# Performance work log

Hardware: AMD Instinct MI355X
Metric: run time of the kernel (lower is better)

Reference implementation:

```python
import jax, jax.numpy as jnp
import numpy as np

SFREQ = 100
NPERSEG = 100  # min(n_times=200, 100)
NOVERLAP = NPERSEG // 2

# periodic hann window (scipy get_window('hann', N) with sym=False)
_WIN_NP = 0.5 - 0.5 * np.cos(2.0 * np.pi * np.arange(NPERSEG) / NPERSEG)
_WIN_SQ_SUM = float(np.sum(_WIN_NP ** 2))
_FREQS = np.fft.rfftfreq(NPERSEG, 1.0 / SFREQ)  # 0..50 Hz, 51 bins
_BANDS = [(0.5, 4.0), (4.0, 8.0), (8.0, 13.0), (13.0, 30.0)]  # delta/theta/alpha/beta
_BAND_IDX = [np.where((_FREQS >= lo) & (_FREQS <= hi))[0] for lo, hi in _BANDS]


def welch_band_features(x):
    """Batched Welch PSD band powers. x: (B,C,T) -> (B, C*4)."""
    B, C, T = x.shape
    step = NPERSEG - NOVERLAP
    n_seg = (T - NPERSEG) // step + 1
    seg_idx = np.arange(n_seg)[:, None] * step + np.arange(NPERSEG)  # (S, L)
    segs = x[..., seg_idx]                              # (B,C,S,L)
    segs = segs - segs.mean(-1, keepdims=True)          # detrend='constant'
    win = jnp.asarray(_WIN_NP, x.dtype)
    spec = jnp.fft.rfft(segs * win, axis=-1)            # (B,C,S,F)
    scale = 1.0 / (SFREQ * _WIN_SQ_SUM)
    psd = (spec.real ** 2 + spec.imag ** 2) * scale
    psd = psd.at[..., 1:-1].multiply(2.0)               # one-sided, nfft even
    psd = psd.mean(-2)                                  # average over segments -> (B,C,F)
    feats = jnp.stack([psd[..., idx].mean(-1) for idx in _BAND_IDX], axis=-1)  # (B,C,4)
    return feats.reshape(B, C * 4)


def setup_inputs() -> dict:
    key = jax.random.key(0)
    ks = jax.random.split(key, 16)
    B, C, T = 2048, 129, 200
    red = C // 8  # 16
    s = 0.05
    inp = {
        "x": jax.random.normal(ks[0], (B, C, T), jnp.float32),
        # channel attention fc (no bias)
        "w_att1": jax.random.normal(ks[1], (C, red), jnp.float32) * s,
        "w_att2": jax.random.normal(ks[2], (red, C), jnp.float32) * s,
        # stand-in EEGNeX backbone: time-mean pool + linear C->64
        "w_bb": jax.random.normal(ks[3], (C, 64), jnp.float32) * s,
        "b_bb": jnp.zeros((64,), jnp.float32),
        # freq encoder
        "w_fe1": jax.random.normal(ks[4], (C * 4, 128), jnp.float32) * s,
        "b_fe1": jnp.zeros((128,), jnp.float32),
        "w_fe2": jax.random.normal(ks[5], (128, 64), jnp.float32) * s,
        "b_fe2": jnp.zeros((64,), jnp.float32),
        # head
        "w_h1": jax.random.normal(ks[6], (128, 128), jnp.float32) * s,
        "b_h1": jnp.zeros((128,), jnp.float32),
        "w_h2": jax.random.normal(ks[7], (128, 64), jnp.float32) * s,
        "b_h2": jnp.zeros((64,), jnp.float32),
        "w_h3": jax.random.normal(ks[8], (64, 1), jnp.float32) * s,
        "b_h3": jnp.zeros((1,), jnp.float32),
    }
    return inp


def reference(x, w_att1, w_att2, w_bb, b_bb, w_fe1, b_fe1, w_fe2, b_fe2,
              w_h1, b_h1, w_h2, b_h2, w_h3, b_h3):
    # --- channel attention ---
    avg = x.mean(-1)                                    # (B,C)
    mx = x.max(-1)                                      # (B,C)
    fc = lambda v: jax.nn.relu(v @ w_att1) @ w_att2
    att = jax.nn.sigmoid(fc(avg) + fc(mx))[..., None]   # (B,C,1)
    x_att = x * att
    # --- backbone (stand-in for EEGNeXBase): time pool + linear ---
    time_feat = jax.nn.relu(x_att.mean(-1) @ w_bb + b_bb)  # (B,64)
    # --- frequency branch (computed from raw x, detached in original) ---
    freq = welch_band_features(jax.lax.stop_gradient(x))   # (B, C*4)
    freq = jax.nn.relu(freq @ w_fe1 + b_fe1)
    freq = jax.nn.relu(freq @ w_fe2 + b_fe2)               # (B,64)
    # --- head ---
    h = jnp.concatenate([time_feat, freq], axis=1)         # (B,128)
    h = jax.nn.relu(h @ w_h1 + b_h1)
    h = jax.nn.relu(h @ w_h2 + b_h2)
    return h @ w_h3 + b_h3                                  # (B,1)
```

## Files before the change

kernel.cpp:

```cpp
#include <hip/hip_runtime.h>
#include <math.h>

constexpr int BB = 2048;
constexpr int CC = 129;
constexpr int TT = 200;
constexpr int NPAIR = BB * CC;
constexpr int PPB = 64;
constexpr int XSTR = 204;

constexpr int OFF_AVG = 8192;
constexpr int OFF_MX  = OFF_AVG + NPAIR;
constexpr int OFF_FT  = OFF_MX + NPAIR;

typedef __bf16 bf16x8 __attribute__((ext_vector_type(8)));
typedef float  f32x4  __attribute__((ext_vector_type(4)));

union BFU { int4 v; bf16x8 b; };
union BSU { __bf16 b; unsigned short u; };

__global__ void kInit(unsigned short* __restrict__ bfr) {
    int tid = blockIdx.x * 256 + threadIdx.x;
    if (tid >= 16384) return;
    int i    = tid & 7;
    int lane = (tid >> 3) & 63;
    int h    = (tid >> 9) & 1;
    int nt   = (tid >> 10) & 3;
    int ks   = tid >> 12;
    int k = ks * 32 + (lane >> 4) * 8 + i;
    int n = nt * 16 + (lane & 15);
    float v = 0.f;
    if (k < 100) {
        if (n < 60) {
            int kb = (n >> 1) + 1;
            const float C = 0.06283185307179587f;
            float w = 0.5f - 0.5f * cosf(C * (float)k);
            int ph = (kb * k) % 100;
            float ang = C * (float)ph;
            v = w * ((n & 1) ? sinf(ang) : cosf(ang));
        } else if (n == 60) {
            v = 0.01f;
        }
    }
    __bf16 hb = (__bf16)v;
    BSU out;
    if (h == 0) out.b = hb;
    else        out.b = (__bf16)(v - (float)hb);
    bfr[tid] = out.u;
}

__global__ __launch_bounds__(256, 2) void kA(const float* __restrict__ x,
                                             const unsigned short* __restrict__ bfr,
                                             float* __restrict__ avg,
                                             float* __restrict__ mxg,
                                             float* __restrict__ feat) {
    __shared__ __align__(16) float xs[PPB * XSTR + 32];

    const int tid = threadIdx.x;
    const int blk = blockIdx.x;

    {
        const float4* xg = (const float4*)(x + (size_t)blk * PPB * TT);
        #pragma unroll
        for (int it = 0; it < 13; it++) {
            int idx = tid + it * 256;
            if (idx < 3200) {
                float4 v = xg[idx];
                int p = idx / 50, t4 = (idx % 50) * 4;
                *(float4*)(xs + p * XSTR + t4) = v;
            }
        }
        if (tid < 64) *(float4*)(xs + tid * XSTR + 200) = float4{0.f, 0.f, 0.f, 0.f};
        if (tid < 32) xs[PPB * XSTR + tid] = 0.f;
    }

    bf16x8 Bh[4][4], Bl[4][4];
    {
        const int4* bg = (const int4*)bfr;
        int ln = tid & 63;
        #pragma unroll
        for (int ks = 0; ks < 4; ks++)
            #pragma unroll
            for (int nt = 0; nt < 4; nt++) {
                BFU uh, ul;
                uh.v = bg[((ks * 4 + nt) * 2 + 0) * 64 + ln];
                ul.v = bg[((ks * 4 + nt) * 2 + 1) * 64 + ln];
                Bh[ks][nt] = uh.b;
                Bl[ks][nt] = ul.b;
            }
    }
    __syncthreads();

    {
        int p = tid >> 2, q = tid & 3;
        const float* src = xs + p * XSTR + q * 50;
        float m = -3.4e38f;
        #pragma unroll
        for (int i = 0; i < 25; i++) {
            float2 v = *(const float2*)(src + i * 2);
            m = fmaxf(m, fmaxf(v.x, v.y));
        }
        m = fmaxf(m, __shfl_xor(m, 1, 64));
        m = fmaxf(m, __shfl_xor(m, 2, 64));
        if (q == 0) mxg[blk * PPB + p] = m;
    }

    const int wv = tid >> 6, lane = tid & 63;
    const int quad = lane >> 4, mrow = lane & 15;
    f32x4 acc[3][4];
    #pragma unroll
    for (int a = 0; a < 3; a++)
        #pragma unroll
        for (int b = 0; b < 4; b++) acc[a][b] = f32x4{0.f, 0.f, 0.f, 0.f};

    #pragma unroll
    for (int mi = 0; mi < 3; mi++) {
        int mt = wv * 3 + mi;
        int r = mt * 16 + mrow;
        int pair = r / 3;
        int seg = r - pair * 3;
        const float* abase = xs + pair * XSTR + seg * 50 + quad * 8;
        #pragma unroll
        for (int ks = 0; ks < 4; ks++) {
            const float* s = abase + ks * 32;
            float2 f0 = *(const float2*)(s);
            float2 f1 = *(const float2*)(s + 2);
            float2 f2 = *(const float2*)(s + 4);
            float2 f3 = *(const float2*)(s + 6);
            float f[8] = {f0.x, f0.y, f1.x, f1.y, f2.x, f2.y, f3.x, f3.y};
            bf16x8 Ah, Al;
            #pragma unroll
            for (int i = 0; i < 8; i++) {
                __bf16 hb = (__bf16)f[i];
                Ah[i] = hb;
                Al[i] = (__bf16)(f[i] - (float)hb);
            }
            #pragma unroll
            for (int nt = 0; nt < 4; nt++) {
                acc[mi][nt] = __builtin_amdgcn_mfma_f32_16x16x32_bf16(Al, Bh[ks][nt], acc[mi][nt], 0, 0, 0);
                acc[mi][nt] = __builtin_amdgcn_mfma_f32_16x16x32_bf16(Ah, Bl[ks][nt], acc[mi][nt], 0, 0, 0);
                acc[mi][nt] = __builtin_amdgcn_mfma_f32_16x16x32_bf16(Ah, Bh[ks][nt], acc[mi][nt], 0, 0, 0);
            }
        }
    }
    __syncthreads();

    float* sp = xs;
    #pragma unroll
    for (int mi = 0; mi < 3; mi++) {
        int mt = wv * 3 + mi;
        #pragma unroll
        for (int nt = 0; nt < 4; nt++) {
            int col = nt * 16 + mrow;
            #pragma unroll
            for (int i = 0; i < 4; i++) {
                int row = mt * 16 + quad * 4 + i;
                sp[row * 66 + col] = acc[mi][nt][i];
            }
        }
    }
    __syncthreads();

    {
        int p = tid >> 2, bnd = tid & 3;
        const int c0[4] = {0, 6, 14, 24};
        const int c1[4] = {7, 15, 25, 59};
        float sum = 0.f;
        #pragma unroll
        for (int s = 0; s < 3; s++) {
            const float* row = sp + (p * 3 + s) * 66;
            float mu = row[60];
            int lo = c0[bnd];
            if (bnd == 0) {
                float v = row[0] + 25.f * mu;
                sum += v * v;
                lo = 1;
            }
            for (int c = lo; c <= c1[bnd]; c++) {
                float v = row[c];
                sum += v * v;
            }
        }
        if (bnd == 0)
            avg[blk * PPB + p] = (sp[(p * 3) * 66 + 60] + sp[(p * 3 + 2) * 66 + 60]) * 0.5f;
        const float cnt[4] = {4.f, 5.f, 6.f, 18.f};
        feat[(size_t)(blk * PPB + p) * 4 + bnd] = sum * (2.f / (11250.f * cnt[bnd]));
    }
}

__global__ __launch_bounds__(256, 8) void kB(const float* __restrict__ avg,
                                             const float* __restrict__ mxv,
                                             const float* __restrict__ feat,
                                             const float* __restrict__ w_att1,
                                             const float* __restrict__ w_att2,
                                             const float* __restrict__ w_bb,
                                             const float* __restrict__ b_bb,
                                             const float* __restrict__ w_fe1,
                                             const float* __restrict__ b_fe1,
                                             const float* __restrict__ w_fe2,
                                             const float* __restrict__ b_fe2,
                                             const float* __restrict__ w_h1,
                                             const float* __restrict__ b_h1,
                                             const float* __restrict__ w_h2,
                                             const float* __restrict__ b_h2,
                                             const float* __restrict__ w_h3,
                                             const float* __restrict__ b_h3,
                                             float* __restrict__ out) {
    __shared__ float s_avg[132], s_mx[132], s_fq[520];
    __shared__ float s_t1a[16], s_t1b[16], s_t1[16];
    __shared__ float s_v[132];
    __shared__ float s_tf[2][64];
    __shared__ float s_p1[2][128];
    __shared__ float s_f1[128];
    __shared__ float s_p2[4][64];
    __shared__ float s_h[128];
    __shared__ float s_pg1[2][128];
    __shared__ float s_g1[128];
    __shared__ float s_pg2[4][64];

    const int b = blockIdx.x;
    const int tid = threadIdx.x;

    for (int i = tid; i < 129; i += 256) { s_avg[i] = avg[b * 129 + i]; s_mx[i] = mxv[b * 129 + i]; }
    for (int i = tid; i < 516; i += 256) s_fq[i] = feat[(size_t)b * 516 + i];
    __syncthreads();

    if (tid < 32) {
        int h = tid & 15;
        const float* src = (tid >= 16) ? s_mx : s_avg;
        float acc = 0.f;
        #pragma unroll 4
        for (int c = 0; c < 129; c++) acc += src[c] * w_att1[c * 16 + h];
        ((tid >= 16) ? s_t1b : s_t1a)[h] = fmaxf(acc, 0.f);
    }
    __syncthreads();
    if (tid < 16) s_t1[tid] = s_t1a[tid] + s_t1b[tid];
    __syncthreads();

    if (tid < 129) {
        float l = 0.f;
        #pragma unroll
        for (int j = 0; j < 16; j++) l += s_t1[j] * w_att2[j * 129 + tid];
        s_v[tid] = s_avg[tid] / (1.f + expf(-l));
    }
    __syncthreads();

    if (tid < 128) {
        int o = tid & 63, ks = tid >> 6;
        int i0 = ks ? 65 : 0, i1 = ks ? 129 : 65;
        float acc = 0.f;
        #pragma unroll 4
        for (int i = i0; i < i1; i++) acc += s_v[i] * w_bb[i * 64 + o];
        s_tf[ks][o] = acc;
    }
    {
        int o = tid & 127, ks = tid >> 7;
        float acc = 0.f;
        #pragma unroll 4
        for (int i = ks * 258; i < ks * 258 + 258; i++) acc += s_fq[i] * w_fe1[i * 128 + o];
        s_p1[ks][o] = acc;
    }
    __syncthreads();
    if (tid < 64) s_h[tid] = fmaxf(s_tf[0][tid] + s_tf[1][tid] + b_bb[tid], 0.f);
    if (tid >= 128) { int o = tid - 128; s_f1[o] = fmaxf(s_p1[0][o] + s_p1[1][o] + b_fe1[o], 0.f); }
    __syncthreads();

    {
        int o = tid & 63, ks = tid >> 6;
        float acc = 0.f;
        #pragma unroll 4
        for (int i = ks * 32; i < ks * 32 + 32; i++) acc += s_f1[i] * w_fe2[i * 64 + o];
        s_p2[ks][o] = acc;
    }
    __syncthreads();
    if (tid < 64) s_h[64 + tid] = fmaxf(s_p2[0][tid] + s_p2[1][tid] + s_p2[2][tid] + s_p2[3][tid] + b_fe2[tid], 0.f);
    __syncthreads();

    {
        int o = tid & 127, ks = tid >> 7;
        float acc = 0.f;
        #pragma unroll 4
        for (int i = ks * 64; i < ks * 64 + 64; i++) acc += s_h[i] * w_h1[i * 128 + o];
        s_pg1[ks][o] = acc;
    }
    __syncthreads();
    if (tid < 128) s_g1[tid] = fmaxf(s_pg1[0][tid] + s_pg1[1][tid] + b_h1[tid], 0.f);
    __syncthreads();

    {
        int o = tid & 63, ks = tid >> 6;
        float acc = 0.f;
        #pragma unroll 4
        for (int i = ks * 32; i < ks * 32 + 32; i++) acc += s_g1[i] * w_h2[i * 64 + o];
        s_pg2[ks][o] = acc;
    }
    __syncthreads();

    if (tid < 64) {
        float g2 = fmaxf(s_pg2[0][tid] + s_pg2[1][tid] + s_pg2[2][tid] + s_pg2[3][tid] + b_h2[tid], 0.f);
        float pz = g2 * w_h3[tid];
        for (int off = 32; off >= 1; off >>= 1) pz += __shfl_xor(pz, off, 64);
        if (tid == 0) out[b] = pz + b_h3[0];
    }
}

extern "C" void kernel_launch(void* const* d_in, const int* in_sizes, int n_in,
                              void* d_out, int out_size, void* d_ws, size_t ws_size,
                              hipStream_t stream) {
    const float* x      = (const float*)d_in[0];
    const float* w_att1 = (const float*)d_in[1];
    const float* w_att2 = (const float*)d_in[2];
    const float* w_bb   = (const float*)d_in[3];
    const float* b_bb   = (const float*)d_in[4];
    const float* w_fe1  = (const float*)d_in[5];
    const float* b_fe1  = (const float*)d_in[6];
    const float* w_fe2  = (const float*)d_in[7];
    const float* b_fe2  = (const float*)d_in[8];
    const float* w_h1   = (const float*)d_in[9];
    const float* b_h1   = (const float*)d_in[10];
    const float* w_h2   = (const float*)d_in[11];
    const float* b_h2   = (const float*)d_in[12];
    const float* w_h3   = (const float*)d_in[13];
    const float* b_h3   = (const float*)d_in[14];

    float* ws = (float*)d_ws;
    unsigned short* bfr = (unsigned short*)ws;
    float* avg = ws + OFF_AVG;
    float* mxv = ws + OFF_MX;
    float* feat = ws + OFF_FT;

    kInit<<<64, 256, 0, stream>>>(bfr);
    kA<<<NPAIR / PPB, 256, 0, stream>>>(x, bfr, avg, mxv, feat);
    kB<<<BB, 256, 0, stream>>>(avg, mxv, feat,
                               w_att1, w_att2, w_bb, b_bb,
                               w_fe1, b_fe1, w_fe2, b_fe2,
                               w_h1, b_h1, w_h2, b_h2, w_h3, b_h3,
                               (float*)d_out);
}
```

Measured before the change: 478.5 us.

## Make kA wave-independent with per-wave LDS slices and no block barriers

```diff
diff --git a/kernel.cpp b/kernel.cpp
--- a/kernel.cpp
+++ b/kernel.cpp
@@ -7,6 +7,7 @@
 constexpr int NPAIR = BB * CC;
 constexpr int PPB = 64;
 constexpr int XSTR = 204;
+constexpr int WSLICE = 16 * XSTR;
 
 constexpr int OFF_AVG = 8192;
 constexpr int OFF_MX  = OFF_AVG + NPAIR;
@@ -48,85 +49,90 @@
     bfr[tid] = out.u;
 }
 
-__global__ __launch_bounds__(256, 2) void kA(const float* __restrict__ x,
+__global__ __launch_bounds__(256, 3) void kA(const float* __restrict__ x,
                                              const unsigned short* __restrict__ bfr,
                                              float* __restrict__ avg,
                                              float* __restrict__ mxg,
                                              float* __restrict__ feat) {
-    __shared__ __align__(16) float xs[PPB * XSTR + 32];
-
-    const int tid = threadIdx.x;
-    const int blk = blockIdx.x;
-
-    {
-        const float4* xg = (const float4*)(x + (size_t)blk * PPB * TT);
-        #pragma unroll
-        for (int it = 0; it < 13; it++) {
-            int idx = tid + it * 256;
-            if (idx < 3200) {
-                float4 v = xg[idx];
-                int p = idx / 50, t4 = (idx % 50) * 4;
-                *(float4*)(xs + p * XSTR + t4) = v;
-            }
-        }
-        if (tid < 64) *(float4*)(xs + tid * XSTR + 200) = float4{0.f, 0.f, 0.f, 0.f};
-        if (tid < 32) xs[PPB * XSTR + tid] = 0.f;
-    }
-
-    bf16x8 Bh[4][4], Bl[4][4];
-    {
-        const int4* bg = (const int4*)bfr;
-        int ln = tid & 63;
-        #pragma unroll
-        for (int ks = 0; ks < 4; ks++)
-            #pragma unroll
-            for (int nt = 0; nt < 4; nt++) {
-                BFU uh, ul;
-                uh.v = bg[((ks * 4 + nt) * 2 + 0) * 64 + ln];
-                ul.v = bg[((ks * 4 + nt) * 2 + 1) * 64 + ln];
-                Bh[ks][nt] = uh.b;
-                Bl[ks][nt] = ul.b;
-            }
-    }
-    __syncthreads();
-
-    {
-        int p = tid >> 2, q = tid & 3;
-        const float* src = xs + p * XSTR + q * 50;
+    __shared__ __align__(16) float xs[4 * WSLICE];
+
+    const int tid  = threadIdx.x;
+    const int blk  = blockIdx.x;
+    const int wv   = tid >> 6;
+    const int lane = tid & 63;
+
+    float* wx = xs + wv * WSLICE;
+
+    {
+        const int p = lane >> 2, q = lane & 3;
+        const float* rowg = x + ((size_t)blk * PPB + wv * 16 + p) * TT;
+        float* rowl = wx + p * XSTR;
         float m = -3.4e38f;
         #pragma unroll
-        for (int i = 0; i < 25; i++) {
-            float2 v = *(const float2*)(src + i * 2);
-            m = fmaxf(m, fmaxf(v.x, v.y));
+        for (int j = 0; j < 13; j++) {
+            int i4 = q + 4 * j;
+            if (i4 < 50) {
+                float4 v = *(const float4*)(rowg + i4 * 4);
+                *(float4*)(rowl + i4 * 4) = v;
+                m = fmaxf(fmaxf(m, fmaxf(v.x, v.y)), fmaxf(v.z, v.w));
+            }
         }
         m = fmaxf(m, __shfl_xor(m, 1, 64));
         m = fmaxf(m, __shfl_xor(m, 2, 64));
-        if (q == 0) mxg[blk * PPB + p] = m;
-    }
-
-    const int wv = tid >> 6, lane = tid & 63;
+        if (q == 0) mxg[blk * PPB + wv * 16 + p] = m;
+    }
+
     const int quad = lane >> 4, mrow = lane & 15;
+
+    const float* abase[3];
+    {
+        #pragma unroll
+        for (int mi = 0; mi < 3; mi++) {
+            int lr = mi * 16 + mrow;
+            int pl = lr / 3;
+            int sg = lr - pl * 3;
+            abase[mi] = wx + pl * XSTR + sg * 50;
+        }
+    }
+
     f32x4 acc[3][4];
     #pragma unroll
     for (int a = 0; a < 3; a++)
         #pragma unroll
         for (int b = 0; b < 4; b++) acc[a][b] = f32x4{0.f, 0.f, 0.f, 0.f};
 
+    const int4* bg = (const int4*)bfr;
     #pragma unroll
-    for (int mi = 0; mi < 3; mi++) {
-        int mt = wv * 3 + mi;
-        int r = mt * 16 + mrow;
-        int pair = r / 3;
-        int seg = r - pair * 3;
-        const float* abase = xs + pair * XSTR + seg * 50 + quad * 8;
-        #pragma unroll
-        for (int ks = 0; ks < 4; ks++) {
-            const float* s = abase + ks * 32;
-            float2 f0 = *(const float2*)(s);
-            float2 f1 = *(const float2*)(s + 2);
-            float2 f2 = *(const float2*)(s + 4);
-            float2 f3 = *(const float2*)(s + 6);
-            float f[8] = {f0.x, f0.y, f1.x, f1.y, f2.x, f2.y, f3.x, f3.y};
+    for (int ks = 0; ks < 4; ks++) {
+        bf16x8 Bh[4], Bl[4];
+        #pragma unroll
+        for (int nt = 0; nt < 4; nt++) {
+            BFU uh, ul;
+            uh.v = bg[((ks * 4 + nt) * 2 + 0) * 64 + lane];
+            ul.v = bg[((ks * 4 + nt) * 2 + 1) * 64 + lane];
+            Bh[nt] = uh.b;
+            Bl[nt] = ul.b;
+        }
+        #pragma unroll
+        for (int mi = 0; mi < 3; mi++) {
+            float f[8];
+            if (ks < 3) {
+                const float* s = abase[mi] + quad * 8 + ks * 32;
+                float2 f0 = *(const float2*)(s);
+                float2 f1 = *(const float2*)(s + 2);
+                float2 f2 = *(const float2*)(s + 4);
+                float2 f3 = *(const float2*)(s + 6);
+                f[0] = f0.x; f[1] = f0.y; f[2] = f1.x; f[3] = f1.y;
+                f[4] = f2.x; f[5] = f2.y; f[6] = f3.x; f[7] = f3.y;
+            } else {
+                const float* s = abase[mi] + 96;
+                float2 f0 = *(const float2*)(s);
+                float2 f1 = *(const float2*)(s + 2);
+                bool v0 = (quad == 0);
+                f[0] = v0 ? f0.x : 0.f; f[1] = v0 ? f0.y : 0.f;
+                f[2] = v0 ? f1.x : 0.f; f[3] = v0 ? f1.y : 0.f;
+                f[4] = 0.f; f[5] = 0.f; f[6] = 0.f; f[7] = 0.f;
+            }
             bf16x8 Ah, Al;
             #pragma unroll
             for (int i = 0; i < 8; i++) {
@@ -134,56 +140,65 @@
                 Ah[i] = hb;
                 Al[i] = (__bf16)(f[i] - (float)hb);
             }
+            __builtin_amdgcn_s_setprio(1);
             #pragma unroll
             for (int nt = 0; nt < 4; nt++) {
-                acc[mi][nt] = __builtin_amdgcn_mfma_f32_16x16x32_bf16(Al, Bh[ks][nt], acc[mi][nt], 0, 0, 0);
-                acc[mi][nt] = __builtin_amdgcn_mfma_f32_16x16x32_bf16(Ah, Bl[ks][nt], acc[mi][nt], 0, 0, 0);
-                acc[mi][nt] = __builtin_amdgcn_mfma_f32_16x16x32_bf16(Ah, Bh[ks][nt], acc[mi][nt], 0, 0, 0);
-            }
-        }
-    }
-    __syncthreads();
-
-    float* sp = xs;
+                acc[mi][nt] = __builtin_amdgcn_mfma_f32_16x16x32_bf16(Al, Bh[nt], acc[mi][nt], 0, 0, 0);
+                acc[mi][nt] = __builtin_amdgcn_mfma_f32_16x16x32_bf16(Ah, Bl[nt], acc[mi][nt], 0, 0, 0);
+                acc[mi][nt] = __builtin_amdgcn_mfma_f32_16x16x32_bf16(Ah, Bh[nt], acc[mi][nt], 0, 0, 0);
+            }
+            __builtin_amdgcn_s_setprio(0);
+        }
+    }
+
+    float* sp = wx;
     #pragma unroll
-    for (int mi = 0; mi < 3; mi++) {
-        int mt = wv * 3 + mi;
+    for (int mi = 0; mi < 3; mi++)
         #pragma unroll
         for (int nt = 0; nt < 4; nt++) {
             int col = nt * 16 + mrow;
             #pragma unroll
-            for (int i = 0; i < 4; i++) {
-                int row = mt * 16 + quad * 4 + i;
-                sp[row * 66 + col] = acc[mi][nt][i];
-            }
-        }
-    }
-    __syncthreads();
-
-    {
-        int p = tid >> 2, bnd = tid & 3;
-        const int c0[4] = {0, 6, 14, 24};
-        const int c1[4] = {7, 15, 25, 59};
-        float sum = 0.f;
-        #pragma unroll
-        for (int s = 0; s < 3; s++) {
-            const float* row = sp + (p * 3 + s) * 66;
+            for (int i = 0; i < 4; i++)
+                sp[(mi * 16 + quad * 4 + i) * 66 + col] = acc[mi][nt][i];
+        }
+
+    {
+        const int p2 = lane >> 2, q = lane & 3;
+        const float* r0 = sp + p2 * 3 * 66;
+        float s0 = 0.f, s1 = 0.f, s2 = 0.f, s3 = 0.f;
+        float mu0 = 0.f, mu2 = 0.f;
+        #pragma unroll
+        for (int sg = 0; sg < 3; sg++) {
+            const float* row = r0 + sg * 66;
             float mu = row[60];
-            int lo = c0[bnd];
-            if (bnd == 0) {
-                float v = row[0] + 25.f * mu;
-                sum += v * v;
-                lo = 1;
-            }
-            for (int c = lo; c <= c1[bnd]; c++) {
+            if (sg == 0) mu0 = mu;
+            if (sg == 2) mu2 = mu;
+            #pragma unroll
+            for (int j = 0; j < 15; j++) {
+                int c = q * 15 + j;
                 float v = row[c];
-                sum += v * v;
-            }
-        }
-        if (bnd == 0)
-            avg[blk * PPB + p] = (sp[(p * 3) * 66 + 60] + sp[(p * 3 + 2) * 66 + 60]) * 0.5f;
-        const float cnt[4] = {4.f, 5.f, 6.f, 18.f};
-        feat[(size_t)(blk * PPB + p) * 4 + bnd] = sum * (2.f / (11250.f * cnt[bnd]));
+                if (j == 0) v = (q == 0) ? (v + 25.f * mu) : v;
+                float v2 = v * v;
+                s0 += (c <= 7) ? v2 : 0.f;
+                s1 += (c >= 6 && c <= 15) ? v2 : 0.f;
+                s2 += (c >= 14 && c <= 25) ? v2 : 0.f;
+                s3 += (c >= 24) ? v2 : 0.f;
+            }
+        }
+        s0 += __shfl_xor(s0, 1, 64); s1 += __shfl_xor(s1, 1, 64);
+        s2 += __shfl_xor(s2, 1, 64); s3 += __shfl_xor(s3, 1, 64);
+        s0 += __shfl_xor(s0, 2, 64); s1 += __shfl_xor(s1, 2, 64);
+        s2 += __shfl_xor(s2, 2, 64); s3 += __shfl_xor(s3, 2, 64);
+        if (q == 0) {
+            int pg = blk * PPB + wv * 16 + p2;
+            float4 fo;
+            fo.x = s0 * (2.f / (11250.f * 4.f));
+            fo.y = s1 * (2.f / (11250.f * 5.f));
+            fo.z = s2 * (2.f / (11250.f * 6.f));
+            fo.w = s3 * (2.f / (11250.f * 18.f));
+            *(float4*)(feat + (size_t)pg * 4) = fo;
+            avg[pg] = (mu0 + mu2) * 0.5f;
+        }
     }
 }
 
```

After: 419.3 us. -12.4%, faster.
